# Kernel tuning notes

Hardware: AMD Instinct MI355X
Metric: run time of the kernel (lower is better)

## Reference

```python
import jax, jax.numpy as jnp
import numpy as np

B, C, D, H, W = 2, 16, 16, 128, 128
CO = 16            # out_channels
C8 = max(C // 8, 1)  # q/k channel dim in CC_module
EPS = 1e-5


def conv3d(x, w, pad):
    # x: [B,C,D,H,W], w: [O,I,kd,kh,kw]
    return jax.lax.conv_general_dilated(
        x, w, (1, 1, 1), [(p, p) for p in pad],
        dimension_numbers=('NCDHW', 'OIDHW', 'NCDHW'))


def bn5d(x, g, b, m, v):
    # eval-mode BatchNorm3d over channel axis 1
    sh = (1, -1, 1, 1, 1)
    return (x - m.reshape(sh)) * (g / jnp.sqrt(v + EPS)).reshape(sh) + b.reshape(sh)


def cc_attention(x, wq, wk, wv, gamma):
    # Criss-cross attention on one depth slice. x: [B,C,H,W]
    q = jnp.einsum('oc,bchw->bohw', wq, x)   # [B,C8,H,W]
    k = jnp.einsum('oc,bchw->bohw', wk, x)   # [B,C8,H,W]
    v = jnp.einsum('oc,bchw->bohw', wv, x)   # [B,C,H,W]
    Hh = x.shape[2]
    # column (H) attention energies, diagonal masked with -inf (CCNet INF trick)
    eH = jnp.einsum('bchw,bcjw->bhwj', q, k)                 # [B,H,W,H]
    eye = jnp.eye(Hh, dtype=bool)[None, :, None, :]
    eH = jnp.where(eye, -jnp.inf, eH)
    # row (W) attention energies
    eW = jnp.einsum('bchw,bchv->bhwv', q, k)                 # [B,H,W,W]
    att = jax.nn.softmax(jnp.concatenate([eH, eW], axis=-1), axis=-1)
    aH, aW = att[..., :Hh], att[..., Hh:]
    oH = jnp.einsum('bhwj,bcjw->bchw', aH, v)
    oW = jnp.einsum('bhwv,bchv->bchw', aW, v)
    return gamma * (oH + oW) + x


def setup_inputs() -> dict:
    key = jax.random.key(0)
    ks = jax.random.split(key, 12)
    f = lambda k, shp, s=0.05: jax.random.normal(k, shp, jnp.float32) * s
    return {
        'x': jax.random.normal(ks[0], (B, C, D, H, W), jnp.float32),
        # Conv3dBNReLU (k=(1,3,3), p=(0,1,1))
        'w_pre': f(ks[1], (C, C, 1, 3, 3)),
        'bn_pre_g': jnp.ones((C,), jnp.float32),
        'bn_pre_b': jnp.zeros((C,), jnp.float32),
        'bn_pre_m': f(ks[2], (C,)),
        'bn_pre_v': jax.random.uniform(ks[3], (C,), jnp.float32, 0.5, 1.5),
        # CC_module params (1x1 convs as matrices)
        'w_q': f(ks[4], (C8, C), 0.2),
        'w_k': f(ks[5], (C8, C), 0.2),
        'w_v': f(ks[6], (C, C), 0.2),
        'cc_gamma': jnp.asarray(0.1, jnp.float32),
        # gate conv BasicConv3d: C -> 4*CO, k=3,s=1,p=1, conv+BN
        'w_gate': f(ks[7], (4 * CO, C, 3, 3, 3)),
        'bn_g': jnp.ones((4 * CO,), jnp.float32),
        'bn_b': jnp.zeros((4 * CO,), jnp.float32),
        'bn_m': f(ks[8], (4 * CO,)),
        'bn_v': jax.random.uniform(ks[9], (4 * CO,), jnp.float32, 0.5, 1.5),
    }


def reference(x, w_pre, bn_pre_g, bn_pre_b, bn_pre_m, bn_pre_v,
              w_q, w_k, w_v, cc_gamma,
              w_gate, bn_g, bn_b, bn_m, bn_v):
    # Conv3dBNReLU
    x = jax.nn.relu(bn5d(conv3d(x, w_pre, (0, 1, 1)),
                         bn_pre_g, bn_pre_b, bn_pre_m, bn_pre_v))
    # criss-cross attention applied twice per depth slice (j in range(2))
    cc2 = lambda xs: cc_attention(
        cc_attention(xs, w_q, w_k, w_v, cc_gamma), w_q, w_k, w_v, cc_gamma)
    x = jax.vmap(cc2, in_axes=2, out_axes=2)(x)
    # SRU gates: conv to 4*CO channels, BN, split, nonlinearities
    gates = bn5d(conv3d(x, w_gate, (1, 1, 1)), bn_g, bn_b, bn_m, bn_v)
    Wx, ft, rt, X = jnp.split(gates, 4, axis=1)
    Wx = jnp.tanh(Wx)
    ft = jax.nn.sigmoid(ft)
    rt = jax.nn.sigmoid(rt)
    X = jnp.tanh(X)  # act == 'tanh'
    # recurrence over depth axis via scan
    Wx_s, ft_s, rt_s, X_s = (jnp.moveaxis(t, 2, 0) for t in (Wx, ft, rt, X))
    C0 = 1.0 - ft_s[0]                        # first step: Ct = 1 - ft
    h0 = rt_s[0] * C0 + (1.0 - rt_s[0]) * X_s[0]

    def step(Ct, inp):
        wx_, ft_, rt_, x_ = inp
        Ct = ft_ * Ct + (1.0 - ft_) * wx_
        ht = rt_ * Ct + (1.0 - rt_) * x_
        return Ct, ht

    _, hts = jax.lax.scan(step, C0, (Wx_s[1:], ft_s[1:], rt_s[1:], X_s[1:]))
    hts = jnp.concatenate([h0[None], hts], axis=0)  # [D,B,CO,H,W]
    return jnp.moveaxis(hts, 0, 2)                  # [B,CO,D,H,W]
```

## Files before the change

### kernel.cpp

```cpp
#include <hip/hip_runtime.h>
#include <math.h>

namespace {
constexpr int B = 2, C = 16, D = 16, H = 128, W = 128;
constexpr int HW   = H * W;
constexpr int DHW  = D * HW;
constexpr int CDHW = C * DHW;
constexpr float EPSBN = 1e-5f;

constexpr long long OFF_R0  = 0;
constexpr long long OFF_R1  = 8388608;
constexpr long long OFF_K   = 16777216;
constexpr long long OFF_KT  = 17825792;
constexpr long long OFF_QT  = 18874368;
constexpr long long OFF_MST = 19922944;
constexpr long long OFF_SO  = 20447232;
constexpr long long OFF_R2  = 20971520;
constexpr long long OFF_R3  = 29360128;
}

using frag_ab = __attribute__((ext_vector_type(8))) short;
using frag_cd = __attribute__((ext_vector_type(4))) float;

__device__ __forceinline__ unsigned short f2bf(float f) {
  unsigned u = __float_as_uint(f);
  u = (u + 0x7FFF + ((u >> 16) & 1)) >> 16;
  return (unsigned short)u;
}
__device__ __forceinline__ float bf2f(short s) {
  return __uint_as_float(((unsigned)(unsigned short)s) << 16);
}
__device__ __forceinline__ unsigned cvt_pk_bf16(float lo, float hi) {
  unsigned r;
  asm volatile("v_cvt_pk_bf16_f32 %0, %1, %2" : "=v"(r) : "v"(lo), "v"(hi));
  return r;
}

__global__ __launch_bounds__(256) void k_x16(
    const float* __restrict__ x, short* __restrict__ XB0)
{
  const int tid = threadIdx.x;
  const int tile = blockIdx.x, d = blockIdx.y, b = blockIdx.z;
  const int h0 = (tile >> 3) * 16, w0 = (tile & 7) * 16;
  const long long xbase = (long long)b * CDHW + (long long)d * HW;
  const int th = tid >> 4, tw = tid & 15;

  float v[16];
  #pragma unroll
  for (int c = 0; c < 16; ++c)
    v[c] = x[xbase + (long long)c * DHW + (h0 + th) * 128 + (w0 + tw)];

  unsigned pk[8];
  #pragma unroll
  for (int c = 0; c < 8; ++c)
    pk[c] = (unsigned)f2bf(v[2 * c]) | ((unsigned)f2bf(v[2 * c + 1]) << 16);
  short* dst = XB0 + ((long long)(b * D + d) * HW + (h0 + th) * 128 + (w0 + tw)) * 16;
  *(uint4*)(dst)     = make_uint4(pk[0], pk[1], pk[2], pk[3]);
  *(uint4*)(dst + 8) = make_uint4(pk[4], pk[5], pk[6], pk[7]);
}

__global__ __launch_bounds__(256) void k_wp(
    const float* __restrict__ wp, short* __restrict__ WP16)
{
  const int idx = blockIdx.x * 256 + threadIdx.x;
  if (idx >= 16 * 160) return;
  const int co = idx / 160;
  const int k = idx - co * 160;
  const int tap = k >> 4, cin = k & 15;
  float v = (tap < 9) ? wp[co * 144 + cin * 9 + tap] : 0.f;
  WP16[idx] = (short)f2bf(v);
}

__global__ __launch_bounds__(256) void k_conv_pre16(
    const short* __restrict__ XB0, const short* __restrict__ WP16,
    const float* __restrict__ bg, const float* __restrict__ bb,
    const float* __restrict__ bm, const float* __restrict__ bv,
    float* __restrict__ X1)
{
  __shared__ short xls[10 * 132 * 16];
  const int tid = threadIdx.x;
  const int rg = blockIdx.x;
  const int d = blockIdx.y, b = blockIdx.z;
  const int h0 = rg * 8;

  const int lane = tid & 63;
  const int wv   = tid >> 6;
  const int p    = lane & 15;
  const int chunk = lane >> 4;

  const short* xb0 = XB0 + (long long)(b * D + d) * HW * 16;
  const frag_ab zero8 = {0, 0, 0, 0, 0, 0, 0, 0};
  for (int idx = tid; idx < 2640; idx += 256) {
    const int pos = idx >> 1, half = idx & 1;
    const int row = pos / 132, col = pos - row * 132;
    const int gh = h0 - 1 + row, gw = col - 1;
    frag_ab v = zero8;
    if (gh >= 0 && gh < H && gw >= 0 && gw < W)
      v = *(const frag_ab*)(xb0 + ((long long)gh * 128 + gw) * 16 + half * 8);
    *(frag_ab*)&xls[(row * 132 + col) * 16 + half * 8] = v;
  }

  frag_ab a[5];
  {
    const short* wl = WP16 + p * 160 + chunk * 8;
    #pragma unroll
    for (int s = 0; s < 5; ++s)
      a[s] = *(const frag_ab*)(wl + s * 32);
  }

  int offs[5];
  #pragma unroll
  for (int s = 0; s < 5; ++s) {
    int tap = 2 * s + (chunk >> 1);
    if (tap > 8) tap = 0;
    const int kh = tap / 3, kw = tap - kh * 3;
    offs[s] = ((2 * wv + kh) * 132 + p + kw) * 16 + (chunk & 1) * 8;
  }

  frag_cd acc[2][8];
  #pragma unroll
  for (int r2 = 0; r2 < 2; ++r2)
    #pragma unroll
    for (int pg = 0; pg < 8; ++pg)
      acc[r2][pg] = (frag_cd){0.f, 0.f, 0.f, 0.f};

  __syncthreads();

  #pragma unroll
  for (int s = 0; s < 5; ++s) {
    const frag_ab av = a[s];
    const int base0 = offs[s];
    #pragma unroll
    for (int pg = 0; pg < 8; ++pg) {
      frag_ab b0 = *(const frag_ab*)&xls[base0 + pg * 256];
      acc[0][pg] = __builtin_amdgcn_mfma_f32_16x16x32_bf16(av, b0, acc[0][pg], 0, 0, 0);
      frag_ab b1 = *(const frag_ab*)&xls[base0 + 2112 + pg * 256];
      acc[1][pg] = __builtin_amdgcn_mfma_f32_16x16x32_bf16(av, b1, acc[1][pg], 0, 0, 0);
    }
  }

  float sc4[4], bi4[4];
  #pragma unroll
  for (int reg = 0; reg < 4; ++reg) {
    const int co = chunk * 4 + reg;
    float s = bg[co] * rsqrtf(bv[co] + EPSBN);
    sc4[reg] = s;
    bi4[reg] = bb[co] - bm[co] * s;
  }
  const long long xbase = (long long)b * CDHW + (long long)d * HW;
  #pragma unroll
  for (int r2 = 0; r2 < 2; ++r2) {
    const int row = h0 + 2 * wv + r2;
    #pragma unroll
    for (int pg = 0; pg < 8; ++pg)
      #pragma unroll
      for (int reg = 0; reg < 4; ++reg) {
        const int co = chunk * 4 + reg;
        float v = fmaxf(fmaf(acc[r2][pg][reg], sc4[reg], bi4[reg]), 0.f);
        X1[xbase + (long long)co * DHW + row * 128 + pg * 16 + p] = v;
      }
  }
}

__global__ __launch_bounds__(256) void k_qkv(
    const float* __restrict__ xin, const float* __restrict__ wq,
    const float* __restrict__ wk, const float* __restrict__ wv,
    float* __restrict__ Kp, float* __restrict__ KTp, float* __restrict__ QTp,
    short* __restrict__ Vp16, short* __restrict__ VTp16)
{
  const int tid = threadIdx.x;
  const int tile = blockIdx.x, d = blockIdx.y, b = blockIdx.z;
  const int h0 = (tile >> 3) * 16, w0 = (tile & 7) * 16;
  const int ty = tid >> 4, tx = tid & 15;
  const int h = h0 + ty, w = w0 + tx;

  const float* xb = xin + (long long)b * CDHW + (long long)d * HW + h * 128 + w;
  float xv[16];
  #pragma unroll
  for (int c = 0; c < 16; ++c) xv[c] = xb[(long long)c * DHW];

  float q0 = 0, q1 = 0, k0 = 0, k1 = 0, v[16];
  #pragma unroll
  for (int c = 0; c < 16; ++c) {
    q0 = fmaf(wq[c], xv[c], q0);
    q1 = fmaf(wq[16 + c], xv[c], q1);
    k0 = fmaf(wk[c], xv[c], k0);
    k1 = fmaf(wk[16 + c], xv[c], k1);
  }
  #pragma unroll
  for (int o = 0; o < 16; ++o) {
    float a = 0;
    #pragma unroll
    for (int c = 0; c < 16; ++c) a = fmaf(wv[o * 16 + c], xv[c], a);
    v[o] = a;
  }

  const int sl = b * 16 + d;
  const long long base2 = (long long)(sl * 2) * HW;
  const long long baseV = (long long)(sl * 16) * HW;
  const int hw = h * 128 + w;
  Kp[base2 + hw] = k0;
  Kp[base2 + HW + hw] = k1;
  #pragma unroll
  for (int o = 0; o < 16; ++o)
    Vp16[baseV + (long long)o * HW + hw] = (short)f2bf(v[o]);

  __shared__ float lsk[2][16][17];
  __shared__ float lsq[2][16][17];
  __shared__ float lsv[16][16][17];
  lsk[0][ty][tx] = k0; lsk[1][ty][tx] = k1;
  lsq[0][ty][tx] = q0; lsq[1][ty][tx] = q1;
  #pragma unroll
  for (int o = 0; o < 16; ++o) lsv[o][ty][tx] = v[o];
  __syncthreads();

  const int wh = (w0 + ty) * 128 + (h0 + tx);
  KTp[base2 + wh]      = lsk[0][tx][ty];
  KTp[base2 + HW + wh] = lsk[1][tx][ty];
  QTp[base2 + wh]      = lsq[0][tx][ty];
  QTp[base2 + HW + wh] = lsq[1][tx][ty];
  #pragma unroll
  for (int o = 0; o < 16; ++o)
    VTp16[baseV + (long long)o * HW + wh] = (short)f2bf(lsv[o][tx][ty]);
}

template<bool MASK_INNER>
__global__ __launch_bounds__(256) void k_att_row(
    const float* __restrict__ xin, float* __restrict__ OWn,
    const float* __restrict__ Kp, const short* __restrict__ Vp16,
    float* __restrict__ Sip, const float* __restrict__ wq)
{
  __shared__ float kr2[4][128][2];
  __shared__ float q0l[4][128], q1l[4][128];
  __shared__ __align__(16) short v16[4][16][136];
  const int tid = threadIdx.x;
  const int o0 = blockIdx.x * 4, d = blockIdx.y, b = blockIdx.z;
  const int sl = b * 16 + d;
  const long long base2 = (long long)(sl * 2) * HW;
  const long long baseV = (long long)(sl * 16) * HW;
  const long long baseM = (long long)sl * HW;
  const int hi = tid >> 6;
  const int L  = tid & 63;
  const int p  = L & 15;
  const int chunk = L >> 4;
  const int orow = o0 + hi;
  const long long xbase = (long long)b * CDHW + (long long)d * HW;

  for (int kk = tid; kk < 1024; kk += 256) {
    int col = kk & 127;
    int t = kk >> 7;
    int r2 = t >> 1, o = t & 1;
    kr2[r2][col][o] = Kp[base2 + (long long)o * HW + (o0 + r2) * 128 + col];
  }
  for (int idx = tid; idx < 2048; idx += 256) {
    int v4 = idx & 31;
    int t = idx >> 5;
    int c = t & 15, r2 = t >> 4;
    *(uint2*)&v16[r2][c][v4 * 4] =
        *(const uint2*)&Vp16[baseV + (long long)c * HW + (o0 + r2) * 128 + v4 * 4];
  }
  {
    float q0a = 0.f, q0b = 0.f, q1a = 0.f, q1b = 0.f;
    #pragma unroll
    for (int c = 0; c < 16; ++c) {
      const float w0 = wq[c], w1 = wq[16 + c];
      float xa = xin[xbase + (long long)c * DHW + orow * 128 + L];
      float xb2 = xin[xbase + (long long)c * DHW + orow * 128 + L + 64];
      q0a = fmaf(w0, xa, q0a);  q1a = fmaf(w1, xa, q1a);
      q0b = fmaf(w0, xb2, q0b); q1b = fmaf(w1, xb2, q1b);
    }
    q0l[hi][L] = q0a; q0l[hi][L + 64] = q0b;
    q1l[hi][L] = q1a; q1l[hi][L + 64] = q1b;
  }
  __syncthreads();

  float q0r[8], q1r[8];
  #pragma unroll
  for (int ti = 0; ti < 8; ++ti) {
    q0r[ti] = q0l[hi][ti * 16 + p];
    q1r[ti] = q1l[hi][ti * 16 + p];
  }

  frag_cd acc[8];
  #pragma unroll
  for (int ti = 0; ti < 8; ++ti) acc[ti] = (frag_cd){0.f, 0.f, 0.f, 0.f};
  float ssum[8] = {0.f, 0.f, 0.f, 0.f, 0.f, 0.f, 0.f, 0.f};

  #pragma unroll
  for (int ks = 0; ks < 4; ++ks) {
    const int vb = ks * 32 + chunk * 8;
    float2 kv[8];
    const float* kvp = &kr2[hi][vb][0];
    *(float4*)&kv[0] = *(const float4*)(kvp);
    *(float4*)&kv[2] = *(const float4*)(kvp + 4);
    *(float4*)&kv[4] = *(const float4*)(kvp + 8);
    *(float4*)&kv[6] = *(const float4*)(kvp + 12);
    frag_ab bfrag = *(const frag_ab*)&v16[hi][p][vb];

    #pragma unroll
    for (int ti = 0; ti < 8; ++ti) {
      float pv[8];
      #pragma unroll
      for (int j = 0; j < 8; ++j) {
        float e = fmaf(q0r[ti], kv[j].x, q1r[ti] * kv[j].y);
        pv[j] = __expf(e);
      }
      if constexpr (MASK_INNER) {
        const int dj = ti * 16 + p - vb;
        #pragma unroll
        for (int j = 0; j < 8; ++j)
          if (j == dj) pv[j] = 0.f;
      }
      float lsum = 0.f;
      #pragma unroll
      for (int j = 0; j < 8; ++j) lsum += pv[j];
      ssum[ti] += lsum;

      union { frag_ab f; unsigned u[4]; } cv;
      cv.u[0] = cvt_pk_bf16(pv[0], pv[1]);
      cv.u[1] = cvt_pk_bf16(pv[2], pv[3]);
      cv.u[2] = cvt_pk_bf16(pv[4], pv[5]);
      cv.u[3] = cvt_pk_bf16(pv[6], pv[7]);
      acc[ti] = __builtin_amdgcn_mfma_f32_16x16x32_bf16(cv.f, bfrag, acc[ti], 0, 0, 0);
    }
  }

  #pragma unroll
  for (int ti = 0; ti < 8; ++ti) {
    ssum[ti] += __shfl_xor(ssum[ti], 16);
    ssum[ti] += __shfl_xor(ssum[ti], 32);
  }
  if (L < 16) {
    #pragma unroll
    for (int ti = 0; ti < 8; ++ti)
      Sip[baseM + (ti * 16 + L) * 128 + orow] = ssum[ti];
  }

  float* ob = OWn + ((long long)(b * D + d) * HW + orow * 128) * 16;
  #pragma unroll
  for (int ti = 0; ti < 8; ++ti)
    #pragma unroll
    for (int reg = 0; reg < 4; ++reg)
      ob[(ti * 16 + chunk * 4 + reg) * 16 + p] = acc[ti][reg];
}

template<bool MASK_INNER>
__global__ __launch_bounds__(256) void k_att_col(
    const float* __restrict__ KTp, const float* __restrict__ QTp,
    const short* __restrict__ VTp16, float* __restrict__ OHn,
    float* __restrict__ Sop)
{
  __shared__ float kr2[4][128][2];
  __shared__ __align__(16) short v16[4][16][136];
  const int tid = threadIdx.x;
  const int i0 = blockIdx.x * 4, d = blockIdx.y, b = blockIdx.z;
  const int sl = b * 16 + d;
  const long long base2 = (long long)(sl * 2) * HW;
  const long long baseV = (long long)(sl * 16) * HW;
  const long long baseS = (long long)sl * HW;
  const int hi = tid >> 6;
  const int L  = tid & 63;
  const int p  = L & 15;
  const int chunk = L >> 4;
  const int icol = i0 + hi;

  for (int kk = tid; kk < 1024; kk += 256) {
    int col = kk & 127;
    int t = kk >> 7;
    int r2 = t >> 1, o = t & 1;
    kr2[r2][col][o] = KTp[base2 + (long long)o * HW + (i0 + r2) * 128 + col];
  }
  for (int idx = tid; idx < 2048; idx += 256) {
    int j4 = idx & 31;
    int t = idx >> 5;
    int c = t & 15, r2 = t >> 4;
    *(uint2*)&v16[r2][c][j4 * 4] =
        *(const uint2*)&VTp16[baseV + (long long)c * HW + (i0 + r2) * 128 + j4 * 4];
  }
  __syncthreads();

  float q0r[8], q1r[8];
  #pragma unroll
  for (int ti = 0; ti < 8; ++ti) {
    q0r[ti] = QTp[base2 + icol * 128 + ti * 16 + p];
    q1r[ti] = QTp[base2 + HW + icol * 128 + ti * 16 + p];
  }

  frag_cd acc[8];
  #pragma unroll
  for (int ti = 0; ti < 8; ++ti) acc[ti] = (frag_cd){0.f, 0.f, 0.f, 0.f};
  float ssum[8] = {0.f, 0.f, 0.f, 0.f, 0.f, 0.f, 0.f, 0.f};

  #pragma unroll
  for (int ks = 0; ks < 4; ++ks) {
    const int vb = ks * 32 + chunk * 8;
    float2 kv[8];
    const float* kvp = &kr2[hi][vb][0];
    *(float4*)&kv[0] = *(const float4*)(kvp);
    *(float4*)&kv[2] = *(const float4*)(kvp + 4);
    *(float4*)&kv[4] = *(const float4*)(kvp + 8);
    *(float4*)&kv[6] = *(const float4*)(kvp + 12);
    frag_ab bfrag = *(const frag_ab*)&v16[hi][p][vb];

    #pragma unroll
    for (int ti = 0; ti < 8; ++ti) {
      float pv[8];
      #pragma unroll
      for (int j = 0; j < 8; ++j) {
        float e = fmaf(q0r[ti], kv[j].x, q1r[ti] * kv[j].y);
        pv[j] = __expf(e);
      }
      if constexpr (!MASK_INNER) {
        const int dj = ti * 16 + p - vb;
        #pragma unroll
        for (int j = 0; j < 8; ++j)
          if (j == dj) pv[j] = 0.f;
      }
      float lsum = 0.f;
      #pragma unroll
      for (int j = 0; j < 8; ++j) lsum += pv[j];
      ssum[ti] += lsum;

      union { frag_ab f; unsigned u[4]; } cv;
      cv.u[0] = cvt_pk_bf16(pv[0], pv[1]);
      cv.u[1] = cvt_pk_bf16(pv[2], pv[3]);
      cv.u[2] = cvt_pk_bf16(pv[4], pv[5]);
      cv.u[3] = cvt_pk_bf16(pv[6], pv[7]);
      acc[ti] = __builtin_amdgcn_mfma_f32_16x16x32_bf16(cv.f, bfrag, acc[ti], 0, 0, 0);
    }
  }

  #pragma unroll
  for (int ti = 0; ti < 8; ++ti) {
    ssum[ti] += __shfl_xor(ssum[ti], 16);
    ssum[ti] += __shfl_xor(ssum[ti], 32);
  }
  if (L < 16) {
    #pragma unroll
    for (int ti = 0; ti < 8; ++ti)
      Sop[baseS + icol * 128 + ti * 16 + L] = ssum[ti];
  }

  float* ob = OHn + ((long long)(b * D + d) * HW + icol * 128) * 16;
  #pragma unroll
  for (int ti = 0; ti < 8; ++ti)
    #pragma unroll
    for (int reg = 0; reg < 4; ++reg)
      ob[(ti * 16 + chunk * 4 + reg) * 16 + p] = acc[ti][reg];
}

template<bool TO_BF16>
__global__ __launch_bounds__(256) void k_comb(
    const float* __restrict__ Xn, const float* __restrict__ OWn,
    const float* __restrict__ OHn, const float* __restrict__ Sip,
    const float* __restrict__ Sop, const float* __restrict__ gp,
    float* __restrict__ Yt, short* __restrict__ Xb16)
{
  __shared__ float xs[16][16][17], ows[16][16][17];
  const int tid = threadIdx.x;
  const int tile = blockIdx.x, d = blockIdx.y, b = blockIdx.z;
  const int o0 = (tile >> 3) * 16, i0 = (tile & 7) * 16;
  const int sl = b * 16 + d;
  const long long baseM = (long long)sl * HW;
  const long long xbase = (long long)b * CDHW + (long long)d * HW;

  const int to = tid >> 4, ti = tid & 15;
  #pragma unroll
  for (int c = 0; c < 16; ++c) {
    const long long src = xbase + (long long)c * DHW + (o0 + to) * 128 + (i0 + ti);
    xs[c][to][ti] = Xn[src];
  }
  {
    const float* osrc = OWn + ((long long)(b * D + d) * HW + (o0 + to) * 128 + (i0 + ti)) * 16;
    float4 f0 = *(const float4*)(osrc);
    float4 f1 = *(const float4*)(osrc + 4);
    float4 f2 = *(const float4*)(osrc + 8);
    float4 f3 = *(const float4*)(osrc + 12);
    ows[0][to][ti] = f0.x;  ows[1][to][ti] = f0.y;
    ows[2][to][ti] = f0.z;  ows[3][to][ti] = f0.w;
    ows[4][to][ti] = f1.x;  ows[5][to][ti] = f1.y;
    ows[6][to][ti] = f1.z;  ows[7][to][ti] = f1.w;
    ows[8][to][ti] = f2.x;  ows[9][to][ti] = f2.y;
    ows[10][to][ti] = f2.z; ows[11][to][ti] = f2.w;
    ows[12][to][ti] = f3.x; ows[13][to][ti] = f3.y;
    ows[14][to][ti] = f3.z; ows[15][to][ti] = f3.w;
  }
  __syncthreads();

  const int ti2 = tid >> 4, to2 = tid & 15;
  const int i = i0 + ti2, o = o0 + to2;
  const float si = Sip[baseM + i * 128 + o];
  const float so = Sop[baseM + i * 128 + o];
  const float gi = gp[0] / (si + so);

  float oh[16];
  {
    const float* osrc = OHn + ((long long)(b * D + d) * HW + i * 128 + o) * 16;
    float4 f0 = *(const float4*)(osrc);
    float4 f1 = *(const float4*)(osrc + 4);
    float4 f2 = *(const float4*)(osrc + 8);
    float4 f3 = *(const float4*)(osrc + 12);
    oh[0] = f0.x;  oh[1] = f0.y;  oh[2] = f0.z;  oh[3] = f0.w;
    oh[4] = f1.x;  oh[5] = f1.y;  oh[6] = f1.z;  oh[7] = f1.w;
    oh[8] = f2.x;  oh[9] = f2.y;  oh[10] = f2.z; oh[11] = f2.w;
    oh[12] = f3.x; oh[13] = f3.y; oh[14] = f3.z; oh[15] = f3.w;
  }

  float res[16];
  #pragma unroll
  for (int c = 0; c < 16; ++c)
    res[c] = fmaf(gi, ows[c][to2][ti2] + oh[c], xs[c][to2][ti2]);

  if constexpr (!TO_BF16) {
    #pragma unroll
    for (int c = 0; c < 16; ++c)
      Yt[xbase + (long long)c * DHW + i * 128 + o] = res[c];
  } else {
    unsigned pk[8];
    #pragma unroll
    for (int c = 0; c < 8; ++c)
      pk[c] = (unsigned)f2bf(res[2 * c]) | ((unsigned)f2bf(res[2 * c + 1]) << 16);
    short* dst = Xb16 + ((long long)(b * D + d) * HW + i * 128 + o) * 16;
    *(uint4*)(dst)     = make_uint4(pk[0], pk[1], pk[2], pk[3]);
    *(uint4*)(dst + 8) = make_uint4(pk[4], pk[5], pk[6], pk[7]);
  }
}

__global__ __launch_bounds__(256) void k_wt(
    const float* __restrict__ wg, short* __restrict__ WT16)
{
  const int idx = blockIdx.x * 256 + threadIdx.x;
  if (idx >= 64 * 448) return;
  const int co_g = idx / 448;
  const int k = idx - co_g * 448;
  const int tap = k >> 4, cin = k & 15;
  float v = (tap < 27) ? wg[co_g * 432 + cin * 27 + tap] : 0.f;
  WT16[idx] = (short)f2bf(v);
}

__global__ __launch_bounds__(256, 2) void k_gates(
    const short* __restrict__ XB16, const short* __restrict__ WT16,
    short* __restrict__ g0, short* __restrict__ g1,
    short* __restrict__ g2, short* __restrict__ g3)
{
  __shared__ short xls[2 * 1584 * 8];
  const int tid = threadIdx.x;
  const int rp = blockIdx.x;
  const int d = blockIdx.y, b = blockIdx.z;
  const int h0 = rp * 2;

  const int lane = tid & 63;
  const int og   = tid >> 6;
  const int p    = lane & 15;
  const int chunk = lane >> 4;

  const short* xb = XB16 + (long long)(b * D) * HW * 16;
  const frag_ab zero8 = {0, 0, 0, 0, 0, 0, 0, 0};
  for (int it = 0; it < 13; ++it) {
    const int ci = it * 256 + tid;
    if (ci < 3168) {
      const int pos = ci >> 1, half = ci & 1;
      const int kd = pos / 528;
      const int rem = pos - kd * 528;
      const int rr = rem / 132;
      const int col = rem - rr * 132;
      const int dd = d - 1 + kd, gh = h0 - 1 + rr, gw = col - 1;
      frag_ab v = zero8;
      if (dd >= 0 && dd < D && gh >= 0 && gh < H && gw >= 0 && gw < W)
        v = *(const frag_ab*)(xb + ((long long)dd * HW + gh * W + gw) * 16 + half * 8);
      *(frag_ab*)&xls[half * 12672 + pos * 8] = v;
    }
  }

  frag_ab a[14];
  {
    const short* wl = WT16 + (og * 16 + p) * 448 + chunk * 8;
    #pragma unroll
    for (int s = 0; s < 14; ++s)
      a[s] = *(const frag_ab*)(wl + s * 32);
  }

  const int t0 = chunk >> 1, half = chunk & 1;
  int offs[14];
  #pragma unroll
  for (int s = 0; s < 14; ++s) {
    int tap = 2 * s + t0;
    if (tap > 26) tap = 0;
    const int kd = (tap * 57) >> 9;
    const int rem = tap - kd * 9;
    const int kh = (rem * 11) >> 5;
    const int kw = rem - kh * 3;
    offs[s] = half * 12672 + ((kd * 4 + kh) * 132 + p + kw) * 8;
  }

  frag_cd acc[2][8];
  #pragma unroll
  for (int r2 = 0; r2 < 2; ++r2)
    #pragma unroll
    for (int pg = 0; pg < 8; ++pg)
      acc[r2][pg] = (frag_cd){0.f, 0.f, 0.f, 0.f};

  __syncthreads();

  #pragma unroll
  for (int s = 0; s < 14; ++s) {
    const frag_ab av = a[s];
    const int base0 = offs[s];
    #pragma unroll
    for (int pg = 0; pg < 8; ++pg) {
      frag_ab b0 = *(const frag_ab*)&xls[base0 + pg * 128];
      acc[0][pg] = __builtin_amdgcn_mfma_f32_16x16x32_bf16(av, b0, acc[0][pg], 0, 0, 0);
      frag_ab b1 = *(const frag_ab*)&xls[base0 + 1056 + pg * 128];
      acc[1][pg] = __builtin_amdgcn_mfma_f32_16x16x32_bf16(av, b1, acc[1][pg], 0, 0, 0);
    }
  }

  short* gbuf = (og == 0) ? g0 : (og == 1) ? g1 : (og == 2) ? g2 : g3;
  const long long base = (long long)b * CDHW + (long long)d * HW + h0 * W;
  #pragma unroll
  for (int r2 = 0; r2 < 2; ++r2)
    #pragma unroll
    for (int pg = 0; pg < 8; ++pg)
      #pragma unroll
      for (int reg = 0; reg < 4; ++reg) {
        const int cc = chunk * 4 + reg;
        gbuf[base + (long long)cc * DHW + r2 * W + pg * 16 + p] =
            (short)f2bf(acc[r2][pg][reg]);
      }
}

__global__ __launch_bounds__(256) void k_scan(
    const short* __restrict__ g0, const short* __restrict__ g1,
    const short* __restrict__ g2, const short* __restrict__ g3,
    const float* __restrict__ bg, const float* __restrict__ bb,
    const float* __restrict__ bm, const float* __restrict__ bv,
    float* __restrict__ out)
{
  const int g = blockIdx.x * 256 + threadIdx.x;
  const int hw = g & 16383;
  const int cc = (g >> 14) & 15;
  const int b  = g >> 18;

  float sc[4], bi[4];
  #pragma unroll
  for (int gg = 0; gg < 4; ++gg) {
    int ch = gg * 16 + cc;
    float s = bg[ch] * rsqrtf(bv[ch] + EPSBN);
    sc[gg] = s;
    bi[gg] = bb[ch] - bm[ch] * s;
  }

  const long long base = (long long)b * CDHW + (long long)cc * DHW + hw;
  float Ct = 0.f;
  for (int d = 0; d < D; ++d) {
    const long long idx = base + (long long)d * HW;
    float wx = tanhf(fmaf(bf2f(g0[idx]), sc[0], bi[0]));
    float ft = 1.f / (1.f + __expf(-fmaf(bf2f(g1[idx]), sc[1], bi[1])));
    float rt = 1.f / (1.f + __expf(-fmaf(bf2f(g2[idx]), sc[2], bi[2])));
    float xg = tanhf(fmaf(bf2f(g3[idx]), sc[3], bi[3]));
    Ct = (d == 0) ? (1.f - ft) : fmaf(ft, Ct, (1.f - ft) * wx);
    out[idx] = fmaf(rt, Ct, (1.f - rt) * xg);
  }
}

extern "C" void kernel_launch(void* const* d_in, const int* in_sizes, int n_in,
                              void* d_out, int out_size, void* d_ws, size_t ws_size,
                              hipStream_t stream) {
  const float* x      = (const float*)d_in[0];
  const float* w_pre  = (const float*)d_in[1];
  const float* bnpg   = (const float*)d_in[2];
  const float* bnpb   = (const float*)d_in[3];
  const float* bnpm   = (const float*)d_in[4];
  const float* bnpv   = (const float*)d_in[5];
  const float* wq     = (const float*)d_in[6];
  const float* wk     = (const float*)d_in[7];
  const float* wv     = (const float*)d_in[8];
  const float* gamma  = (const float*)d_in[9];
  const float* w_gate = (const float*)d_in[10];
  const float* bng    = (const float*)d_in[11];
  const float* bnb    = (const float*)d_in[12];
  const float* bnm    = (const float*)d_in[13];
  const float* bnv    = (const float*)d_in[14];

  float* ws  = (float*)d_ws;
  float* R0  = ws + OFF_R0;
  float* R1  = ws + OFF_R1;
  float* Kb  = ws + OFF_K;
  float* KTb = ws + OFF_KT;
  float* QTb = ws + OFF_QT;
  float* SI  = ws + OFF_MST;
  float* SO  = ws + OFF_SO;
  float* R2  = ws + OFF_R2;
  float* R3  = ws + OFF_R3;
  short* XB0  = (short*)(ws + OFF_R1);
  short* XB16 = (short*)(ws + OFF_R1);
  short* WP16 = (short*)(ws + OFF_SO);
  short* WT16 = (short*)(ws + OFF_K);
  short* V1b  = (short*)(ws + OFF_R2);
  short* VT1b = (short*)(ws + OFF_R3);
  short* V2b  = (short*)(ws + OFF_R0);
  short* VT2b = (short*)(ws + OFF_R1) + 8388608;
  short* G0b = (short*)(ws + OFF_R0);
  short* G1b = (short*)(ws + OFF_R0) + 8388608;
  short* G2b = (short*)(ws + OFF_R2);
  short* G3b = (short*)(ws + OFF_R2) + 8388608;
  float* out = (float*)d_out;

  const dim3 gTile(64, D, B), gAtt(32, D, B);

  k_wp <<<dim3(10),  dim3(256), 0, stream>>>(w_pre, WP16);
  k_x16<<<gTile,     dim3(256), 0, stream>>>(x, XB0);
  k_conv_pre16<<<dim3(16, D, B), dim3(256), 0, stream>>>(
      XB0, WP16, bnpg, bnpb, bnpm, bnpv, R0);

  k_qkv<<<gTile, dim3(256), 0, stream>>>(R0, wq, wk, wv, Kb, KTb, QTb, V1b, VT1b);
  k_att_row<false><<<gAtt, dim3(256), 0, stream>>>(R0, R1, Kb, V1b, SI, wq);
  k_att_col<false><<<gAtt, dim3(256), 0, stream>>>(KTb, QTb, VT1b, R2, SO);
  k_comb<false><<<gTile, dim3(256), 0, stream>>>(R0, R1, R2, SI, SO, gamma, R3, nullptr);

  k_qkv<<<gTile, dim3(256), 0, stream>>>(R3, wq, wk, wv, Kb, KTb, QTb, V2b, VT2b);
  k_att_row<true><<<gAtt, dim3(256), 0, stream>>>(R3, R2, Kb, V2b, SI, wq);
  k_att_col<true><<<gAtt, dim3(256), 0, stream>>>(KTb, QTb, VT2b, R0, SO);
  k_comb<true><<<gTile, dim3(256), 0, stream>>>(R3, R2, R0, SI, SO, gamma, nullptr, XB16);

  k_wt<<<dim3(112), dim3(256), 0, stream>>>(w_gate, WT16);

  k_gates<<<dim3(64, D, B), dim3(256), 0, stream>>>(XB16, WT16, G0b, G1b, G2b, G3b);

  k_scan<<<dim3(2048), dim3(256), 0, stream>>>(G0b, G1b, G2b, G3b, bng, bnb, bnm, bnv, out);
}
```

Measured before the change: 300.8 us.

## Split conv K-loop into two 8-channel halves to halve LDS tile footprint

Both MFMA convolutions (pre conv and gate conv) now stage only 8 input channels at a time in shared memory and loop over two channel halves, with weights re-laid out per half and 4 taps per 32-wide K step. This halves LDS usage per block, which can allow more resident blocks and better latency hiding. In exchange it adds an extra global-load/sync phase per block, and because 2 taps per K step become 4, the gate conv now does 7+7=14 MFMA steps (same) while pre conv goes from 5 to 6 steps, adding some padded work.

```diff
diff --git a/kernel.cpp b/kernel.cpp
--- a/kernel.cpp
+++ b/kernel.cpp
@@ -63,10 +63,14 @@
     const float* __restrict__ wp, short* __restrict__ WP16)
 {
   const int idx = blockIdx.x * 256 + threadIdx.x;
-  if (idx >= 16 * 160) return;
-  const int co = idx / 160;
-  const int k = idx - co * 160;
-  const int tap = k >> 4, cin = k & 15;
+  if (idx >= 2 * 16 * 96) return;
+  const int u = idx / 96;
+  const int k = idx - u * 96;
+  const int ks = k >> 5, rem = k & 31;
+  const int t = rem >> 3, c8 = rem & 7;
+  const int tap = ks * 4 + t;
+  const int half = u >> 4, co = u & 15;
+  const int cin = half * 8 + c8;
   float v = (tap < 9) ? wp[co * 144 + cin * 9 + tap] : 0.f;
   WP16[idx] = (short)f2bf(v);
 }
@@ -77,7 +81,7 @@
     const float* __restrict__ bm, const float* __restrict__ bv,
     float* __restrict__ X1)
 {
-  __shared__ short xls[10 * 132 * 16];
+  __shared__ short xls[10 * 132 * 8];
   const int tid = threadIdx.x;
   const int rg = blockIdx.x;
   const int d = blockIdx.y, b = blockIdx.z;
@@ -90,32 +94,6 @@
 
   const short* xb0 = XB0 + (long long)(b * D + d) * HW * 16;
   const frag_ab zero8 = {0, 0, 0, 0, 0, 0, 0, 0};
-  for (int idx = tid; idx < 2640; idx += 256) {
-    const int pos = idx >> 1, half = idx & 1;
-    const int row = pos / 132, col = pos - row * 132;
-    const int gh = h0 - 1 + row, gw = col - 1;
-    frag_ab v = zero8;
-    if (gh >= 0 && gh < H && gw >= 0 && gw < W)
-      v = *(const frag_ab*)(xb0 + ((long long)gh * 128 + gw) * 16 + half * 8);
-    *(frag_ab*)&xls[(row * 132 + col) * 16 + half * 8] = v;
-  }
-
-  frag_ab a[5];
-  {
-    const short* wl = WP16 + p * 160 + chunk * 8;
-    #pragma unroll
-    for (int s = 0; s < 5; ++s)
-      a[s] = *(const frag_ab*)(wl + s * 32);
-  }
-
-  int offs[5];
-  #pragma unroll
-  for (int s = 0; s < 5; ++s) {
-    int tap = 2 * s + (chunk >> 1);
-    if (tap > 8) tap = 0;
-    const int kh = tap / 3, kw = tap - kh * 3;
-    offs[s] = ((2 * wv + kh) * 132 + p + kw) * 16 + (chunk & 1) * 8;
-  }
 
   frag_cd acc[2][8];
   #pragma unroll
@@ -124,19 +102,48 @@
     for (int pg = 0; pg < 8; ++pg)
       acc[r2][pg] = (frag_cd){0.f, 0.f, 0.f, 0.f};
 
-  __syncthreads();
-
-  #pragma unroll
-  for (int s = 0; s < 5; ++s) {
-    const frag_ab av = a[s];
-    const int base0 = offs[s];
-    #pragma unroll
-    for (int pg = 0; pg < 8; ++pg) {
-      frag_ab b0 = *(const frag_ab*)&xls[base0 + pg * 256];
-      acc[0][pg] = __builtin_amdgcn_mfma_f32_16x16x32_bf16(av, b0, acc[0][pg], 0, 0, 0);
-      frag_ab b1 = *(const frag_ab*)&xls[base0 + 2112 + pg * 256];
-      acc[1][pg] = __builtin_amdgcn_mfma_f32_16x16x32_bf16(av, b1, acc[1][pg], 0, 0, 0);
-    }
+  int offs[3];
+  #pragma unroll
+  for (int s = 0; s < 3; ++s) {
+    int tap = s * 4 + chunk;
+    if (tap > 8) tap = 0;
+    const int kh = (tap * 11) >> 5;
+    const int kw = tap - kh * 3;
+    offs[s] = ((2 * wv + kh) * 132 + p + kw) * 8;
+  }
+
+  for (int half = 0; half < 2; ++half) {
+    for (int idx = tid; idx < 1320; idx += 256) {
+      const int row = idx / 132, col = idx - row * 132;
+      const int gh = h0 - 1 + row, gw = col - 1;
+      frag_ab v = zero8;
+      if (gh >= 0 && gh < H && gw >= 0 && gw < W)
+        v = *(const frag_ab*)(xb0 + ((long long)gh * 128 + gw) * 16 + half * 8);
+      *(frag_ab*)&xls[idx * 8] = v;
+    }
+    __syncthreads();
+
+    frag_ab a[3];
+    {
+      const short* wl = WP16 + ((half << 4) + p) * 96 + chunk * 8;
+      #pragma unroll
+      for (int s = 0; s < 3; ++s)
+        a[s] = *(const frag_ab*)(wl + s * 32);
+    }
+
+    #pragma unroll
+    for (int s = 0; s < 3; ++s) {
+      const frag_ab av = a[s];
+      const int base0 = offs[s];
+      #pragma unroll
+      for (int pg = 0; pg < 8; ++pg) {
+        frag_ab b0 = *(const frag_ab*)&xls[base0 + pg * 128];
+        acc[0][pg] = __builtin_amdgcn_mfma_f32_16x16x32_bf16(av, b0, acc[0][pg], 0, 0, 0);
+        frag_ab b1 = *(const frag_ab*)&xls[base0 + 1056 + pg * 128];
+        acc[1][pg] = __builtin_amdgcn_mfma_f32_16x16x32_bf16(av, b1, acc[1][pg], 0, 0, 0);
+      }
+    }
+    __syncthreads();
   }
 
   float sc4[4], bi4[4];
@@ -530,11 +537,15 @@
     const float* __restrict__ wg, short* __restrict__ WT16)
 {
   const int idx = blockIdx.x * 256 + threadIdx.x;
-  if (idx >= 64 * 448) return;
-  const int co_g = idx / 448;
-  const int k = idx - co_g * 448;
-  const int tap = k >> 4, cin = k & 15;
-  float v = (tap < 27) ? wg[co_g * 432 + cin * 27 + tap] : 0.f;
+  if (idx >= 2 * 64 * 224) return;
+  const int u = idx / 224;
+  const int k = idx - u * 224;
+  const int ks = k >> 5, rem = k & 31;
+  const int t = rem >> 3, c8 = rem & 7;
+  const int tap = ks * 4 + t;
+  const int half = u >> 6, co = u & 63;
+  const int cin = half * 8 + c8;
+  float v = (tap < 27) ? wg[co * 432 + cin * 27 + tap] : 0.f;
   WT16[idx] = (short)f2bf(v);
 }
 
@@ -543,7 +554,7 @@
     short* __restrict__ g0, short* __restrict__ g1,
     short* __restrict__ g2, short* __restrict__ g3)
 {
-  __shared__ short xls[2 * 1584 * 8];
+  __shared__ short xls[1584 * 8];
   const int tid = threadIdx.x;
   const int rp = blockIdx.x;
   const int d = blockIdx.y, b = blockIdx.z;
@@ -556,63 +567,61 @@
 
   const short* xb = XB16 + (long long)(b * D) * HW * 16;
   const frag_ab zero8 = {0, 0, 0, 0, 0, 0, 0, 0};
-  for (int it = 0; it < 13; ++it) {
-    const int ci = it * 256 + tid;
-    if (ci < 3168) {
-      const int pos = ci >> 1, half = ci & 1;
-      const int kd = pos / 528;
-      const int rem = pos - kd * 528;
+
+  frag_cd acc[2][8];
+  #pragma unroll
+  for (int r2 = 0; r2 < 2; ++r2)
+    #pragma unroll
+    for (int pg = 0; pg < 8; ++pg)
+      acc[r2][pg] = (frag_cd){0.f, 0.f, 0.f, 0.f};
+
+  int offs[7];
+  #pragma unroll
+  for (int s = 0; s < 7; ++s) {
+    int tap = s * 4 + chunk;
+    if (tap > 26) tap = 0;
+    const int kd = (tap * 57) >> 9;
+    const int rem = tap - kd * 9;
+    const int kh = (rem * 11) >> 5;
+    const int kw = rem - kh * 3;
+    offs[s] = ((kd * 4 + kh) * 132 + p + kw) * 8;
+  }
+
+  for (int half = 0; half < 2; ++half) {
+    for (int idx = tid; idx < 1584; idx += 256) {
+      const int kd = idx / 528;
+      const int rem = idx - kd * 528;
       const int rr = rem / 132;
       const int col = rem - rr * 132;
       const int dd = d - 1 + kd, gh = h0 - 1 + rr, gw = col - 1;
       frag_ab v = zero8;
       if (dd >= 0 && dd < D && gh >= 0 && gh < H && gw >= 0 && gw < W)
         v = *(const frag_ab*)(xb + ((long long)dd * HW + gh * W + gw) * 16 + half * 8);
-      *(frag_ab*)&xls[half * 12672 + pos * 8] = v;
-    }
-  }
-
-  frag_ab a[14];
-  {
-    const short* wl = WT16 + (og * 16 + p) * 448 + chunk * 8;
-    #pragma unroll
-    for (int s = 0; s < 14; ++s)
-      a[s] = *(const frag_ab*)(wl + s * 32);
-  }
-
-  const int t0 = chunk >> 1, half = chunk & 1;
-  int offs[14];
-  #pragma unroll
-  for (int s = 0; s < 14; ++s) {
-    int tap = 2 * s + t0;
-    if (tap > 26) tap = 0;
-    const int kd = (tap * 57) >> 9;
-    const int rem = tap - kd * 9;
-    const int kh = (rem * 11) >> 5;
-    const int kw = rem - kh * 3;
-    offs[s] = half * 12672 + ((kd * 4 + kh) * 132 + p + kw) * 8;
-  }
-
-  frag_cd acc[2][8];
-  #pragma unroll
-  for (int r2 = 0; r2 < 2; ++r2)
-    #pragma unroll
-    for (int pg = 0; pg < 8; ++pg)
-      acc[r2][pg] = (frag_cd){0.f, 0.f, 0.f, 0.f};
-
-  __syncthreads();
-
-  #pragma unroll
-  for (int s = 0; s < 14; ++s) {
-    const frag_ab av = a[s];
-    const int base0 = offs[s];
-    #pragma unroll
-    for (int pg = 0; pg < 8; ++pg) {
-      frag_ab b0 = *(const frag_ab*)&xls[base0 + pg * 128];
-      acc[0][pg] = __builtin_amdgcn_mfma_f32_16x16x32_bf16(av, b0, acc[0][pg], 0, 0, 0);
-      frag_ab b1 = *(const frag_ab*)&xls[base0 + 1056 + pg * 128];
-      acc[1][pg] = __builtin_amdgcn_mfma_f32_16x16x32_bf16(av, b1, acc[1][pg], 0, 0, 0);
-    }
+      *(frag_ab*)&xls[idx * 8] = v;
+    }
+    __syncthreads();
+
+    frag_ab a[7];
+    {
+      const short* wl = WT16 + ((half << 6) + og * 16 + p) * 224 + chunk * 8;
+      #pragma unroll
+      for (int s = 0; s < 7; ++s)
+        a[s] = *(const frag_ab*)(wl + s * 32);
+    }
+
+    #pragma unroll
+    for (int s = 0; s < 7; ++s) {
+      const frag_ab av = a[s];
+      const int base0 = offs[s];
+      #pragma unroll
+      for (int pg = 0; pg < 8; ++pg) {
+        frag_ab b0 = *(const frag_ab*)&xls[base0 + pg * 128];
+        acc[0][pg] = __builtin_amdgcn_mfma_f32_16x16x32_bf16(av, b0, acc[0][pg], 0, 0, 0);
+        frag_ab b1 = *(const frag_ab*)&xls[base0 + 1056 + pg * 128];
+        acc[1][pg] = __builtin_amdgcn_mfma_f32_16x16x32_bf16(av, b1, acc[1][pg], 0, 0, 0);
+      }
+    }
+    __syncthreads();
   }
 
   short* gbuf = (og == 0) ? g0 : (og == 1) ? g1 : (og == 2) ? g2 : g3;
@@ -708,7 +717,7 @@
 
   const dim3 gTile(64, D, B), gAtt(32, D, B);
 
-  k_wp <<<dim3(10),  dim3(256), 0, stream>>>(w_pre, WP16);
+  k_wp <<<dim3(12),  dim3(256), 0, stream>>>(w_pre, WP16);
   k_x16<<<gTile,     dim3(256), 0, stream>>>(x, XB0);
   k_conv_pre16<<<dim3(16, D, B), dim3(256), 0, stream>>>(
       XB0, WP16, bnpg, bnpb, bnpm, bnpv, R0);
```

Result: no change. 297.8 us, median of 3 (-1.0%).
